# Kernel tuning notes

Hardware: AMD Instinct MI355X
Metric: run time of the kernel (lower is better)

The kernel has to match this reference:

```python
import jax, jax.numpy as jnp
import numpy as np
import math

V, H, L, NH, I, E, K, S, B = 32000, 1024, 4, 16, 2816, 8, 2, 2048, 1
HD = H // NH
MOE_IDX = 2
EPS = 1e-6
THETA = 10000.0
AUX_COEF, Z_COEF = 0.01, 0.001


def setup_inputs() -> dict:
    key = jax.random.key(0)
    ks = jax.random.split(key, 20)
    std = 0.02
    n_dense = L - 1  # layers 0,1,3
    inp = {
        "input_ids": jax.random.randint(ks[0], (B, S), 0, V, dtype=jnp.int64),
        "embed": jax.random.normal(ks[1], (V, H), jnp.float32) * std,
        "ln1_w": jnp.ones((L, H), jnp.float32),
        "ln2_w": jnp.ones((L, H), jnp.float32),
        "wq": jax.random.normal(ks[2], (L, H, H), jnp.float32) * std,
        "wk": jax.random.normal(ks[3], (L, H, H), jnp.float32) * std,
        "wv": jax.random.normal(ks[4], (L, H, H), jnp.float32) * std,
        "wo": jax.random.normal(ks[5], (L, H, H), jnp.float32) * std,
        "dense_gate": jax.random.normal(ks[6], (n_dense, H, I), jnp.float32) * std,
        "dense_up": jax.random.normal(ks[7], (n_dense, H, I), jnp.float32) * std,
        "dense_down": jax.random.normal(ks[8], (n_dense, I, H), jnp.float32) * std,
        "router_w": jax.random.normal(ks[9], (H, E), jnp.float32) * std,
        "moe_gate": jax.random.normal(ks[10], (E, H, I), jnp.float32) * std,
        "moe_up": jax.random.normal(ks[11], (E, H, I), jnp.float32) * std,
        "moe_down": jax.random.normal(ks[12], (E, I, H), jnp.float32) * std,
        "final_norm_w": jnp.ones((H,), jnp.float32),
    }
    return inp


def rmsnorm(x, w):
    return x * jax.lax.rsqrt(jnp.mean(x * x, -1, keepdims=True) + EPS) * w


def rope_tables():
    inv_freq = 1.0 / (THETA ** (jnp.arange(0, HD, 2, dtype=jnp.float32) / HD))
    ang = jnp.arange(S, dtype=jnp.float32)[:, None] * inv_freq[None, :]  # [S, HD/2]
    return jnp.cos(ang), jnp.sin(ang)


def apply_rope(x, cos, sin):
    # x: [B,S,NH,HD]; cos/sin [S,HD/2] -> broadcast [1,S,1,HD/2]
    c = cos[None, :, None, :]
    s = sin[None, :, None, :]
    x1, x2 = jnp.split(x, 2, axis=-1)
    return jnp.concatenate([x1 * c - x2 * s, x2 * c + x1 * s], axis=-1)


def attention(x, wq, wk, wv, wo, cos, sin, mask):
    q = (x @ wq).reshape(B, S, NH, HD)
    k = (x @ wk).reshape(B, S, NH, HD)
    v = (x @ wv).reshape(B, S, NH, HD)
    q = apply_rope(q, cos, sin)
    k = apply_rope(k, cos, sin)
    scores = jnp.einsum("bqhd,bkhd->bhqk", q, k) / math.sqrt(HD)
    scores = jnp.where(mask, scores, jnp.finfo(scores.dtype).min)
    p = jax.nn.softmax(scores, axis=-1)
    o = jnp.einsum("bhqk,bkhd->bqhd", p, v).reshape(B, S, H)
    return o @ wo


def swiglu_mlp(x, wg, wu, wd):
    return (jax.nn.silu(x @ wg) * (x @ wu)) @ wd


def moe_layer(x, router_w, wg, wu, wd):
    T = B * S
    xf = x.reshape(T, H)
    rl = xf @ router_w  # [T,E]
    probs = jax.nn.softmax(rl, axis=-1)
    vals, idx = jax.lax.top_k(probs, K)  # [T,K]
    vals = vals / jnp.sum(vals, axis=-1, keepdims=True)
    rows = jnp.arange(T)[:, None]
    w = jnp.zeros((T, E), xf.dtype).at[rows, idx].set(vals)  # dense combine weights
    g = jnp.einsum("th,ehi->tei", xf, wg)
    u = jnp.einsum("th,ehi->tei", xf, wu)
    a = jax.nn.silu(g) * u
    y = jnp.einsum("tei,eih,te->th", a, wd, w)
    # load-balancing aux loss (Switch-style) + router z-loss
    sel = jnp.zeros((T, E), xf.dtype).at[rows, idx].add(1.0)
    f = jnp.mean(sel, axis=0)
    P = jnp.mean(probs, axis=0)
    aux = AUX_COEF * E * jnp.sum(f * P)
    z = Z_COEF * jnp.mean(jax.nn.logsumexp(rl, axis=-1) ** 2)
    return y.reshape(B, S, H), aux + z


def reference(input_ids, embed, ln1_w, ln2_w, wq, wk, wv, wo,
              dense_gate, dense_up, dense_down,
              router_w, moe_gate, moe_up, moe_down, final_norm_w):
    cos, sin = rope_tables()
    mask = jnp.tril(jnp.ones((S, S), bool))[None, None, :, :]
    h = embed[input_ids]  # [B,S,H]
    total_aux = jnp.float32(0.0)
    n_moe = 0
    d = 0  # dense layer counter
    for li in range(L):
        res = h
        hn = rmsnorm(h, ln1_w[li])
        h = res + attention(hn, wq[li], wk[li], wv[li], wo[li], cos, sin, mask)
        res = h
        hn = rmsnorm(h, ln2_w[li])
        if li == MOE_IDX:
            y, aux = moe_layer(hn, router_w, moe_gate, moe_up, moe_down)
            total_aux = total_aux + aux
            n_moe += 1
        else:
            y = swiglu_mlp(hn, dense_gate[d], dense_up[d], dense_down[d])
            d += 1
        h = res + y
    h = rmsnorm(h, final_norm_w)
    logits = h @ embed.T  # tied lm_head
    aux_loss = total_aux / n_moe
    return logits, aux_loss
```

## Files before the change

kernel.cpp:

```cpp
#include <hip/hip_runtime.h>
#include <hip/hip_bf16.h>
#include <math.h>

#define SEQ 2048
#define HID 1024
#define NHEAD 16
#define HDIM 64
#define IDIM 2816
#define NEXP 8
#define VOCAB 32000

#define ASTRIDE 144

typedef float f32x4v __attribute__((ext_vector_type(4)));
typedef __bf16 bf16x8v __attribute__((ext_vector_type(8)));
typedef __bf16 bf16x4v __attribute__((ext_vector_type(4)));

__device__ __forceinline__ bf16x8v cvt8(const float4& a, const float4& b) {
  bf16x8v r;
  r[0] = (__bf16)a.x; r[1] = (__bf16)a.y; r[2] = (__bf16)a.z; r[3] = (__bf16)a.w;
  r[4] = (__bf16)b.x; r[5] = (__bf16)b.y; r[6] = (__bf16)b.z; r[7] = (__bf16)b.w;
  return r;
}

#define MFMA(a, b, c) __builtin_amdgcn_mfma_f32_16x16x32_bf16(a, b, c, 0, 0, 0)

__device__ __forceinline__ void gld_lds16(const void* g, void* l) {
  __builtin_amdgcn_global_load_lds(
      (const __attribute__((address_space(1))) unsigned int*)(unsigned long long)g,
      (__attribute__((address_space(3))) unsigned int*)(unsigned int)(unsigned long long)l,
      16, 0, 0);
}

__global__ __launch_bounds__(256) void wsplit_t_kernel(
    const float* __restrict__ W, __bf16* __restrict__ WH, __bf16* __restrict__ WL,
    int K, int N)
{
  __shared__ float tile[64][65];
  const int tid = threadIdx.x;
  const size_t zofs = (size_t)blockIdx.z * K * N;
  const int n0 = blockIdx.x * 64, k0 = blockIdx.y * 64;
#pragma unroll
  for (int r = 0; r < 4; ++r) {
    int kk = (tid >> 4) + r * 16;
    int nn = (tid & 15) * 4;
    float4 v = *(const float4*)(W + zofs + (size_t)(k0 + kk) * N + n0 + nn);
    tile[kk][nn] = v.x; tile[kk][nn + 1] = v.y;
    tile[kk][nn + 2] = v.z; tile[kk][nn + 3] = v.w;
  }
  __syncthreads();
  const int nn = tid >> 2;
  const int kk = (tid & 3) * 16;
  __bf16* dh = WH + zofs + (size_t)(n0 + nn) * K + k0 + kk;
  __bf16* dl = WL + zofs + (size_t)(n0 + nn) * K + k0 + kk;
  bf16x8v h0, l0, h1, l1;
#pragma unroll
  for (int j = 0; j < 8; ++j) {
    float f = tile[kk + j][nn];
    __bf16 hb = (__bf16)f; h0[j] = hb; l0[j] = (__bf16)(f - (float)hb);
    f = tile[kk + 8 + j][nn];
    hb = (__bf16)f; h1[j] = hb; l1[j] = (__bf16)(f - (float)hb);
  }
  *(bf16x8v*)dh = h0; *(bf16x8v*)(dh + 8) = h1;
  *(bf16x8v*)dl = l0; *(bf16x8v*)(dl + 8) = l1;
}

__global__ __launch_bounds__(256) void wsplit_th_kernel(
    const float* __restrict__ W, __bf16* __restrict__ WH, int K, int N)
{
  __shared__ float tile[64][65];
  const int tid = threadIdx.x;
  const size_t zofs = (size_t)blockIdx.z * K * N;
  const int n0 = blockIdx.x * 64, k0 = blockIdx.y * 64;
#pragma unroll
  for (int r = 0; r < 4; ++r) {
    int kk = (tid >> 4) + r * 16;
    int nn = (tid & 15) * 4;
    float4 v = *(const float4*)(W + zofs + (size_t)(k0 + kk) * N + n0 + nn);
    tile[kk][nn] = v.x; tile[kk][nn + 1] = v.y;
    tile[kk][nn + 2] = v.z; tile[kk][nn + 3] = v.w;
  }
  __syncthreads();
  const int nn = tid >> 2;
  const int kk = (tid & 3) * 16;
  __bf16* dh = WH + zofs + (size_t)(n0 + nn) * K + k0 + kk;
  bf16x8v h0, h1;
#pragma unroll
  for (int j = 0; j < 8; ++j) {
    h0[j] = (__bf16)tile[kk + j][nn];
    h1[j] = (__bf16)tile[kk + 8 + j][nn];
  }
  *(bf16x8v*)dh = h0; *(bf16x8v*)(dh + 8) = h1;
}

__global__ __launch_bounds__(256) void esplit_kernel(
    const float* __restrict__ E, __bf16* __restrict__ EH)
{
  size_t i = ((size_t)blockIdx.x * 256 + threadIdx.x) * 8;
  float4 a = *(const float4*)(E + i);
  float4 b = *(const float4*)(E + i + 4);
  *(bf16x8v*)(EH + i) = cvt8(a, b);
}

template<bool COMP, bool ACCUM, int BM, int BN, bool XSWZ>
__global__ __launch_bounds__(256) void gemm_bt_kernel(
    const __bf16* __restrict__ Ah, const __bf16* __restrict__ Al,
    const __bf16* __restrict__ B0h, const __bf16* __restrict__ B0l,
    const __bf16* __restrict__ B1h, const __bf16* __restrict__ B1l,
    const __bf16* __restrict__ B2h, const __bf16* __restrict__ B2l,
    float* __restrict__ C0, float* __restrict__ C1, float* __restrict__ C2,
    int M, int N, int Kd)
{
  const __bf16* __restrict__ Bh = (blockIdx.z == 0) ? B0h : (blockIdx.z == 1 ? B1h : B2h);
  const __bf16* __restrict__ Bl = (blockIdx.z == 0) ? B0l : (blockIdx.z == 1 ? B1l : B2l);
  float* __restrict__ C         = (blockIdx.z == 0) ? C0 : (blockIdx.z == 1 ? C1 : C2);
  constexpr int ATILE = BM * 64;
  constexpr int BTILE = BN * 64;
  constexpr int MFR = BM / 32;
  constexpr int NFR = BN / 32;
  __shared__ __align__(16) char smem[COMP ? 2 * (ATILE + BTILE) : (ATILE + BTILE)];
  char* AsH = smem;
  char* BsH = smem + ATILE;
  char* AsL = COMP ? smem + ATILE + BTILE : smem;
  char* BsL = COMP ? smem + 2 * ATILE + BTILE : smem + ATILE;
  const int tid = threadIdx.x;
  int bm, bn;
  if (XSWZ) {
    int id = blockIdx.x;
    int xcd = id & 7;
    int j = id >> 3;
    if (BM == 128) {
      bm = j & 15;
      bn = xcd * 32 + (j >> 4);
    } else {
      bm = j & 31;
      bn = xcd * 32 + (j >> 5);
    }
    if (bn >= N / BN) return;
  } else {
    bm = blockIdx.y;
    bn = blockIdx.x;
  }
  const int wid = tid >> 6, lane = tid & 63;
  const int wm = (wid >> 1) * (BM / 2), wn = (wid & 1) * (BN / 2);
  const int lr = lane & 15, kh = lane >> 4;
  const int lrow = lane >> 2;
  const int lcol = (lane & 3) << 3;

  f32x4v acc[MFR][NFR];
  const f32x4v z4 = {0.f, 0.f, 0.f, 0.f};
#pragma unroll
  for (int i = 0; i < MFR; ++i)
#pragma unroll
    for (int j2 = 0; j2 < NFR; ++j2) acc[i][j2] = z4;

  for (int k0 = 0; k0 < Kd; k0 += 32) {
    __syncthreads();
#pragma unroll
    for (int c = wid; c < BM / 16; c += 4) {
      size_t gofs = (size_t)(bm * BM + c * 16 + lrow) * Kd + k0 + lcol;
      gld_lds16(Ah + gofs, AsH + c * 1024);
      if (COMP) gld_lds16(Al + gofs, AsL + c * 1024);
    }
#pragma unroll
    for (int c = wid; c < BN / 16; c += 4) {
      size_t gofs = (size_t)(bn * BN + c * 16 + lrow) * Kd + k0 + lcol;
      gld_lds16(Bh + gofs, BsH + c * 1024);
      if (COMP) gld_lds16(Bl + gofs, BsL + c * 1024);
    }
    __syncthreads();

    bf16x8v ah[MFR], al[MFR], bh4[NFR], bl4[NFR];
#pragma unroll
    for (int i = 0; i < MFR; ++i) {
      int r = wm + (i << 4) + lr;
      int off = r * 64 + (kh << 4);
      ah[i] = *(const bf16x8v*)(AsH + off);
      if (COMP) al[i] = *(const bf16x8v*)(AsL + off);
    }
#pragma unroll
    for (int i = 0; i < NFR; ++i) {
      int r = wn + (i << 4) + lr;
      int off = r * 64 + (kh << 4);
      bh4[i] = *(const bf16x8v*)(BsH + off);
      if (COMP) bl4[i] = *(const bf16x8v*)(BsL + off);
    }
#pragma unroll
    for (int mi = 0; mi < MFR; ++mi)
#pragma unroll
      for (int ni = 0; ni < NFR; ++ni) {
        if (COMP) {
          acc[mi][ni] = MFMA(al[mi], bh4[ni], acc[mi][ni]);
          acc[mi][ni] = MFMA(ah[mi], bl4[ni], acc[mi][ni]);
        }
        acc[mi][ni] = MFMA(ah[mi], bh4[ni], acc[mi][ni]);
      }
  }

  const int cr0 = kh << 2;
#pragma unroll
  for (int mi = 0; mi < MFR; ++mi)
#pragma unroll
    for (int ni = 0; ni < NFR; ++ni)
#pragma unroll
      for (int r = 0; r < 4; ++r) {
        int row = bm * BM + wm + (mi << 4) + cr0 + r;
        int col = bn * BN + wn + (ni << 4) + lr;
        size_t idx = (size_t)row * N + col;
        if (ACCUM) C[idx] += acc[mi][ni][r];
        else       C[idx] = acc[mi][ni][r];
      }
}

template<bool COMP>
__global__ __launch_bounds__(256) void gemm_qkv_kernel(
    const __bf16* __restrict__ Ah, const __bf16* __restrict__ Al,
    const __bf16* __restrict__ Bqh, const __bf16* __restrict__ Bql,
    const __bf16* __restrict__ Bkh, const __bf16* __restrict__ Bkl,
    const __bf16* __restrict__ Bvh, const __bf16* __restrict__ Bvl,
    __bf16* __restrict__ QH, __bf16* __restrict__ QL,
    __bf16* __restrict__ KH, __bf16* __restrict__ KL,
    float* __restrict__ Vout,
    const float* __restrict__ CT, const float* __restrict__ ST)
{
  const __bf16* __restrict__ Bh = (blockIdx.z == 0) ? Bqh : (blockIdx.z == 1 ? Bkh : Bvh);
  const __bf16* __restrict__ Bl = (blockIdx.z == 0) ? Bql : (blockIdx.z == 1 ? Bkl : Bvl);
  constexpr int ATILE = 64 * 64;
  constexpr int BTILE = 128 * 64;
  __shared__ __align__(16) char smem[COMP ? 2 * (ATILE + BTILE) : (ATILE + BTILE)];
  char* AsH = smem;
  char* BsH = smem + ATILE;
  char* AsL = COMP ? smem + ATILE + BTILE : smem;
  char* BsL = COMP ? smem + 2 * ATILE + BTILE : smem + ATILE;
  const int tid = threadIdx.x;
  const int bm = blockIdx.y, bn = blockIdx.x;
  const int wid = tid >> 6, lane = tid & 63;
  const int wm = (wid >> 1) << 5, wn = (wid & 1) << 6;
  const int lr = lane & 15, kh = lane >> 4;
  const int lrow = lane >> 2;
  const int lcol = (lane & 3) << 3;

  f32x4v acc[2][4];
  const f32x4v z4 = {0.f, 0.f, 0.f, 0.f};
#pragma unroll
  for (int i = 0; i < 2; ++i)
#pragma unroll
    for (int j2 = 0; j2 < 4; ++j2) acc[i][j2] = z4;

  for (int k0 = 0; k0 < HID; k0 += 32) {
    __syncthreads();
    {
      int c = wid;
      size_t gofs = (size_t)(bm * 64 + c * 16 + lrow) * HID + k0 + lcol;
      gld_lds16(Ah + gofs, AsH + c * 1024);
      if (COMP) gld_lds16(Al + gofs, AsL + c * 1024);
    }
#pragma unroll
    for (int c = wid; c < 8; c += 4) {
      size_t gofs = (size_t)(bn * 128 + c * 16 + lrow) * HID + k0 + lcol;
      gld_lds16(Bh + gofs, BsH + c * 1024);
      if (COMP) gld_lds16(Bl + gofs, BsL + c * 1024);
    }
    __syncthreads();

    bf16x8v ah2[2], al2[2], bh4[4], bl4[4];
#pragma unroll
    for (int i = 0; i < 2; ++i) {
      int r = wm + (i << 4) + lr;
      int off = r * 64 + (kh << 4);
      ah2[i] = *(const bf16x8v*)(AsH + off);
      if (COMP) al2[i] = *(const bf16x8v*)(AsL + off);
    }
#pragma unroll
    for (int i = 0; i < 4; ++i) {
      int r = wn + (i << 4) + lr;
      int off = r * 64 + (kh << 4);
      bh4[i] = *(const bf16x8v*)(BsH + off);
      if (COMP) bl4[i] = *(const bf16x8v*)(BsL + off);
    }
#pragma unroll
    for (int mi = 0; mi < 2; ++mi)
#pragma unroll
      for (int ni = 0; ni < 4; ++ni) {
        if (COMP) {
          acc[mi][ni] = MFMA(al2[mi], bh4[ni], acc[mi][ni]);
          acc[mi][ni] = MFMA(ah2[mi], bl4[ni], acc[mi][ni]);
        }
        acc[mi][ni] = MFMA(ah2[mi], bh4[ni], acc[mi][ni]);
      }
  }

  const int cr0 = kh << 2;
  if (blockIdx.z == 2) {
#pragma unroll
    for (int mi = 0; mi < 2; ++mi)
#pragma unroll
      for (int ni = 0; ni < 4; ++ni)
#pragma unroll
        for (int r = 0; r < 4; ++r) {
          int row = bm * 64 + wm + (mi << 4) + cr0 + r;
          int col = bn * 128 + wn + (ni << 4) + lr;
          Vout[(size_t)row * HID + col] = acc[mi][ni][r];
        }
  } else {
    const float scale = (blockIdx.z == 0) ? 0.125f : 1.0f;
    __bf16* OH = (blockIdx.z == 0) ? QH : KH;
    __bf16* OL = (blockIdx.z == 0) ? QL : KL;
#pragma unroll
    for (int mi = 0; mi < 2; ++mi)
#pragma unroll
      for (int ni = 0; ni < 2; ++ni)
#pragma unroll
        for (int r = 0; r < 4; ++r) {
          int row = bm * 64 + wm + (mi << 4) + cr0 + r;
          int col = bn * 128 + wn + (ni << 4) + lr;
          int i = col & 31;
          float c = CT[row * 32 + i], sn = ST[row * 32 + i];
          float x1 = acc[mi][ni][r];
          float x2 = acc[mi][ni + 2][r];
          float o1 = (x1 * c - x2 * sn) * scale;
          float o2 = (x2 * c + x1 * sn) * scale;
          size_t ofs = (size_t)row * HID + col;
          __bf16 h1 = (__bf16)o1;
          OH[ofs] = h1; OL[ofs] = (__bf16)(o1 - (float)h1);
          __bf16 h2 = (__bf16)o2;
          OH[ofs + 32] = h2; OL[ofs + 32] = (__bf16)(o2 - (float)h2);
        }
  }
}

template<bool COMP>
__global__ __launch_bounds__(256) void gemm_dgu_kernel(
    const __bf16* __restrict__ Ah, const __bf16* __restrict__ Al,
    const __bf16* __restrict__ BGh, const __bf16* __restrict__ BGl,
    const __bf16* __restrict__ BUh, const __bf16* __restrict__ BUl,
    __bf16* __restrict__ GH, __bf16* __restrict__ GL)
{
  __shared__ __align__(16) char AsH[4096], AsL[4096];
  __shared__ __align__(16) char BgH[4096], BgL[4096];
  __shared__ __align__(16) char BuH[4096], BuL[4096];
  const int tid = threadIdx.x;
  const int bn = blockIdx.x, bm = blockIdx.y;
  const int wid = tid >> 6, lane = tid & 63;
  const int wm = (wid >> 1) << 5, wn = (wid & 1) << 5;
  const int lr = lane & 15, kh = lane >> 4;
  const int lrow = lane >> 2;
  const int lcol = (lane & 3) << 3;

  f32x4v accg[2][2], accu[2][2];
  const f32x4v z4 = {0.f, 0.f, 0.f, 0.f};
#pragma unroll
  for (int i = 0; i < 2; ++i)
#pragma unroll
    for (int j = 0; j < 2; ++j) { accg[i][j] = z4; accu[i][j] = z4; }

  for (int k0 = 0; k0 < HID; k0 += 32) {
    __syncthreads();
    {
      int c = wid;
      size_t aofs = (size_t)(bm * 64 + c * 16 + lrow) * HID + k0 + lcol;
      gld_lds16(Ah + aofs, AsH + c * 1024);
      if (COMP) gld_lds16(Al + aofs, AsL + c * 1024);
      size_t bofs = (size_t)(bn * 64 + c * 16 + lrow) * HID + k0 + lcol;
      gld_lds16(BGh + bofs, BgH + c * 1024);
      gld_lds16(BUh + bofs, BuH + c * 1024);
      if (COMP) {
        gld_lds16(BGl + bofs, BgL + c * 1024);
        gld_lds16(BUl + bofs, BuL + c * 1024);
      }
    }
    __syncthreads();

    bf16x8v af[2], afl[2], bg4[2], bgl4[2], bu4[2], bul4[2];
#pragma unroll
    for (int i = 0; i < 2; ++i) {
      int r = wm + (i << 4) + lr;
      int off = r * 64 + (kh << 4);
      af[i] = *(const bf16x8v*)(AsH + off);
      if (COMP) afl[i] = *(const bf16x8v*)(AsL + off);
    }
#pragma unroll
    for (int i = 0; i < 2; ++i) {
      int r = wn + (i << 4) + lr;
      int off = r * 64 + (kh << 4);
      bg4[i] = *(const bf16x8v*)(BgH + off);
      bu4[i] = *(const bf16x8v*)(BuH + off);
      if (COMP) {
        bgl4[i] = *(const bf16x8v*)(BgL + off);
        bul4[i] = *(const bf16x8v*)(BuL + off);
      }
    }
#pragma unroll
    for (int mi = 0; mi < 2; ++mi)
#pragma unroll
      for (int ni = 0; ni < 2; ++ni) {
        if (COMP) {
          accg[mi][ni] = MFMA(afl[mi], bg4[ni], accg[mi][ni]);
          accg[mi][ni] = MFMA(af[mi], bgl4[ni], accg[mi][ni]);
        }
        accg[mi][ni] = MFMA(af[mi], bg4[ni], accg[mi][ni]);
        if (COMP) {
          accu[mi][ni] = MFMA(afl[mi], bu4[ni], accu[mi][ni]);
          accu[mi][ni] = MFMA(af[mi], bul4[ni], accu[mi][ni]);
        }
        accu[mi][ni] = MFMA(af[mi], bu4[ni], accu[mi][ni]);
      }
  }

  const int cr0 = kh << 2;
#pragma unroll
  for (int mi = 0; mi < 2; ++mi)
#pragma unroll
    for (int ni = 0; ni < 2; ++ni)
#pragma unroll
      for (int r = 0; r < 4; ++r) {
        int row = bm * 64 + wm + (mi << 4) + cr0 + r;
        int col = bn * 64 + wn + (ni << 4) + lr;
        float gv = accg[mi][ni][r];
        float uv = accu[mi][ni][r];
        float a = gv / (1.f + __expf(-gv)) * uv;
        size_t idx = (size_t)row * IDIM + col;
        __bf16 hb = (__bf16)a;
        GH[idx] = hb;
        GL[idx] = (__bf16)(a - (float)hb);
      }
}

__global__ __launch_bounds__(256) void vtsplit_kernel(
    const float* __restrict__ V, __bf16* __restrict__ VTH, __bf16* __restrict__ VTL)
{
  __shared__ float tile[64][65];
  const int tid = threadIdx.x;
  const int s0 = blockIdx.x * 64;
  const int head = blockIdx.y;
#pragma unroll
  for (int r = 0; r < 4; ++r) {
    int ss = (tid >> 4) + r * 16;
    int dd = (tid & 15) * 4;
    float4 v = *(const float4*)(V + (size_t)(s0 + ss) * HID + head * 64 + dd);
    tile[ss][dd] = v.x; tile[ss][dd + 1] = v.y;
    tile[ss][dd + 2] = v.z; tile[ss][dd + 3] = v.w;
  }
  __syncthreads();
#pragma unroll
  for (int half = 0; half < 2; ++half) {
    const int d = (tid >> 3) + (half << 5);
    const int c = tid & 7;
    bf16x8v hv, lv;
#pragma unroll
    for (int j = 0; j < 8; ++j) {
      float f = tile[c * 8 + j][d];
      __bf16 hb = (__bf16)f;
      hv[j] = hb; lv[j] = (__bf16)(f - (float)hb);
    }
    size_t dst = (size_t)(head * 64 + d) * SEQ + s0 + c * 8;
    *(bf16x8v*)(VTH + dst) = hv;
    *(bf16x8v*)(VTL + dst) = lv;
  }
}

__global__ __launch_bounds__(256) void attn_flash_kernel(
    const __bf16* __restrict__ QH, const __bf16* __restrict__ QL,
    const __bf16* __restrict__ KH, const __bf16* __restrict__ KL,
    const __bf16* __restrict__ VTH, const __bf16* __restrict__ VTL,
    __bf16* __restrict__ OH, __bf16* __restrict__ OL)
{
  const int head = blockIdx.y;
  const int tid = threadIdx.x, wid = tid >> 6, lane = tid & 63;
  const int lr = lane & 15, kh = lane >> 4;
  __shared__ __align__(16) char KsH[64 * ASTRIDE], KsL[64 * ASTRIDE];
  __shared__ __align__(16) char VtH[64 * ASTRIDE], VtL[64 * ASTRIDE];
  __shared__ __align__(16) char PsH[4][16 * ASTRIDE], PsL[4][16 * ASTRIDE];

#pragma unroll
  for (int seg = 0; seg < 2; ++seg) {
    const int qt = seg ? (31 - (int)blockIdx.x) : (int)blockIdx.x;

    const size_t qofs = (size_t)(qt * 64 + wid * 16 + lr) * HID + head * HDIM;
    const bf16x8v qfh0 = *(const bf16x8v*)(QH + qofs + (kh << 3));
    const bf16x8v qfh1 = *(const bf16x8v*)(QH + qofs + 32 + (kh << 3));
    const bf16x8v qfl0 = *(const bf16x8v*)(QL + qofs + (kh << 3));
    const bf16x8v qfl1 = *(const bf16x8v*)(QL + qofs + 32 + (kh << 3));

    float m_run[4], l_run[4];
    f32x4v oacc[4];
    const f32x4v z4 = {0.f, 0.f, 0.f, 0.f};
#pragma unroll
    for (int i = 0; i < 4; ++i) { m_run[i] = -1e30f; l_run[i] = 0.f; oacc[i] = z4; }

    for (int kt = 0; kt <= qt; ++kt) {
      __syncthreads();
#pragma unroll
      for (int p = 0; p < 2; ++p) {
        int g = tid + (p << 8);
        int r = g >> 3;
        int c = g & 7;
        int off = r * ASTRIDE + (c << 4);
        const size_t kofs = (size_t)(kt * 64 + r) * HID + head * HDIM + (c << 3);
        *(bf16x8v*)(KsH + off) = *(const bf16x8v*)(KH + kofs);
        *(bf16x8v*)(KsL + off) = *(const bf16x8v*)(KL + kofs);
        const size_t vofs = (size_t)(head * 64 + r) * SEQ + kt * 64 + (c << 3);
        *(bf16x8v*)(VtH + off) = *(const bf16x8v*)(VTH + vofs);
        *(bf16x8v*)(VtL + off) = *(const bf16x8v*)(VTL + vofs);
      }
      __syncthreads();

      float sv[4][4];
#pragma unroll
      for (int stt = 0; stt < 4; ++stt) {
        int r = (stt << 4) + lr;
        int off0 = r * ASTRIDE + (kh << 4);
        int off1 = off0 + 64;
        bf16x8v kfh0 = *(const bf16x8v*)(KsH + off0);
        bf16x8v kfl0 = *(const bf16x8v*)(KsL + off0);
        bf16x8v kfh1 = *(const bf16x8v*)(KsH + off1);
        bf16x8v kfl1 = *(const bf16x8v*)(KsL + off1);
        f32x4v s = z4;
        s = MFMA(qfl0, kfh0, s);
        s = MFMA(qfh0, kfl0, s);
        s = MFMA(qfh0, kfh0, s);
        s = MFMA(qfl1, kfh1, s);
        s = MFMA(qfh1, kfl1, s);
        s = MFMA(qfh1, kfh1, s);
        int key = kt * 64 + (stt << 4) + lr;
#pragma unroll
        for (int rr = 0; rr < 4; ++rr) {
          int qr = qt * 64 + wid * 16 + (kh << 2) + rr;
          sv[stt][rr] = (key <= qr) ? s[rr] : -1e30f;
        }
      }

#pragma unroll
      for (int rr = 0; rr < 4; ++rr) {
        float mx = fmaxf(fmaxf(sv[0][rr], sv[1][rr]), fmaxf(sv[2][rr], sv[3][rr]));
#pragma unroll
        for (int d = 1; d < 16; d <<= 1) mx = fmaxf(mx, __shfl_xor(mx, d));
        float mnew = fmaxf(m_run[rr], mx);
        float scl = __expf(m_run[rr] - mnew);
        float pv[4];
#pragma unroll
        for (int stt = 0; stt < 4; ++stt) pv[stt] = __expf(sv[stt][rr] - mnew);
        float rs = pv[0] + pv[1] + pv[2] + pv[3];
#pragma unroll
        for (int d = 1; d < 16; d <<= 1) rs += __shfl_xor(rs, d);
        l_run[rr] = l_run[rr] * scl + rs;
        m_run[rr] = mnew;
#pragma unroll
        for (int n = 0; n < 4; ++n) oacc[n][rr] *= scl;
        int qlr = (kh << 2) + rr;
#pragma unroll
        for (int stt = 0; stt < 4; ++stt) {
          __bf16 hb = (__bf16)pv[stt];
          __bf16 lb = (__bf16)(pv[stt] - (float)hb);
          int off = qlr * ASTRIDE + (((stt << 4) + lr) << 1);
          *(__bf16*)(PsH[wid] + off) = hb;
          *(__bf16*)(PsL[wid] + off) = lb;
        }
      }

      int poff0 = lr * ASTRIDE + (kh << 4);
      int poff1 = poff0 + 64;
      bf16x8v pah0 = *(const bf16x8v*)(PsH[wid] + poff0);
      bf16x8v pal0 = *(const bf16x8v*)(PsL[wid] + poff0);
      bf16x8v pah1 = *(const bf16x8v*)(PsH[wid] + poff1);
      bf16x8v pal1 = *(const bf16x8v*)(PsL[wid] + poff1);
#pragma unroll
      for (int n = 0; n < 4; ++n) {
        int vr = (n << 4) + lr;
        int voff0 = vr * ASTRIDE + (kh << 4);
        int voff1 = voff0 + 64;
        bf16x8v vfh0 = *(const bf16x8v*)(VtH + voff0);
        bf16x8v vfl0 = *(const bf16x8v*)(VtL + voff0);
        bf16x8v vfh1 = *(const bf16x8v*)(VtH + voff1);
        bf16x8v vfl1 = *(const bf16x8v*)(VtL + voff1);
        oacc[n] = MFMA(pal0, vfh0, oacc[n]);
        oacc[n] = MFMA(pah0, vfl0, oacc[n]);
        oacc[n] = MFMA(pah0, vfh0, oacc[n]);
        oacc[n] = MFMA(pal1, vfh1, oacc[n]);
        oacc[n] = MFMA(pah1, vfl1, oacc[n]);
        oacc[n] = MFMA(pah1, vfh1, oacc[n]);
      }
    }

#pragma unroll
    for (int n = 0; n < 4; ++n)
#pragma unroll
      for (int rr = 0; rr < 4; ++rr) {
        int qr = qt * 64 + wid * 16 + (kh << 2) + rr;
        size_t ofs = (size_t)qr * HID + head * HDIM + (n << 4) + lr;
        float val = oacc[n][rr] / l_run[rr];
        __bf16 hb = (__bf16)val;
        OH[ofs] = hb;
        OL[ofs] = (__bf16)(val - (float)hb);
      }
  }
}

__global__ __launch_bounds__(256) void gemm_moe_guf_kernel(
    const __bf16* __restrict__ Xh,
    const __bf16* __restrict__ MGH, const __bf16* __restrict__ MUH,
    __bf16* __restrict__ A2, const float* __restrict__ W,
    const int* __restrict__ list, const int* __restrict__ cnt8,
    const int* __restrict__ off8)
{
  const int e = blockIdx.z;
  const int cnt = cnt8[e];
  const int bn = blockIdx.x, bm = blockIdx.y;
  if (bm * 128 >= cnt) return;
  const int base = off8[e];
  __shared__ __align__(16) char AsB[8192];
  __shared__ __align__(16) char BgB[4096];
  __shared__ __align__(16) char BuB[4096];
  const int tid = threadIdx.x;
  const int wid = tid >> 6, lane = tid & 63;
  const int wm = (wid >> 1) << 6, wn = (wid & 1) << 5;
  const int lr = lane & 15, kh = lane >> 4;
  const int lrow = lane >> 2;
  const int lcol = (lane & 3) << 3;

  f32x4v accg[4][2], accu[4][2];
  const f32x4v z4 = {0.f, 0.f, 0.f, 0.f};
#pragma unroll
  for (int i = 0; i < 4; ++i)
#pragma unroll
    for (int j = 0; j < 2; ++j) { accg[i][j] = z4; accu[i][j] = z4; }

  for (int k0 = 0; k0 < HID; k0 += 32) {
    __syncthreads();
#pragma unroll
    for (int c = wid; c < 8; c += 4) {
      int rg = bm * 128 + c * 16 + lrow;
      int tok = list[e * SEQ + (rg < cnt ? rg : cnt - 1)];
      gld_lds16(Xh + (size_t)tok * HID + k0 + lcol, AsB + c * 1024);
    }
    {
      int c = wid;
      size_t wofs = (size_t)(e * IDIM + bn * 64 + c * 16 + lrow) * HID + k0 + lcol;
      gld_lds16(MGH + wofs, BgB + c * 1024);
      gld_lds16(MUH + wofs, BuB + c * 1024);
    }
    __syncthreads();

    bf16x8v af[4], bg4[2], bu4[2];
#pragma unroll
    for (int i = 0; i < 4; ++i) {
      int r = wm + (i << 4) + lr;
      af[i] = *(const bf16x8v*)(AsB + r * 64 + (kh << 4));
    }
#pragma unroll
    for (int i = 0; i < 2; ++i) {
      int r = wn + (i << 4) + lr;
      bg4[i] = *(const bf16x8v*)(BgB + r * 64 + (kh << 4));
      bu4[i] = *(const bf16x8v*)(BuB + r * 64 + (kh << 4));
    }
#pragma unroll
    for (int mi = 0; mi < 4; ++mi)
#pragma unroll
      for (int ni = 0; ni < 2; ++ni) {
        accg[mi][ni] = MFMA(af[mi], bg4[ni], accg[mi][ni]);
        accu[mi][ni] = MFMA(af[mi], bu4[ni], accu[mi][ni]);
      }
  }

  const int cr0 = kh << 2;
#pragma unroll
  for (int mi = 0; mi < 4; ++mi)
#pragma unroll
    for (int ni = 0; ni < 2; ++ni)
#pragma unroll
      for (int r = 0; r < 4; ++r) {
        int row = bm * 128 + wm + (mi << 4) + cr0 + r;
        if (row < cnt) {
          int col = bn * 64 + wn + (ni << 4) + lr;
          int tok = list[e * SEQ + row];
          float w = W[tok * 8 + e];
          float gval = accg[mi][ni][r];
          float uval = accu[mi][ni][r];
          float a = gval / (1.f + __expf(-gval)) * uval * w;
          A2[(size_t)(base + row) * IDIM + col] = (__bf16)a;
        }
      }
}

__global__ __launch_bounds__(256) void gemm_moe_down2_kernel(
    const __bf16* __restrict__ A2, const __bf16* __restrict__ MDH,
    float* __restrict__ Y2,
    const int* __restrict__ cnt8, const int* __restrict__ off8)
{
  const int e = blockIdx.z;
  const int cnt = cnt8[e];
  const int bn = blockIdx.x, bm = blockIdx.y;
  if (bm * 128 >= cnt) return;
  const int base = off8[e];
  __shared__ __align__(16) char AsB[8192];
  __shared__ __align__(16) char BsB[4096];
  const int tid = threadIdx.x;
  const int wid = tid >> 6, lane = tid & 63;
  const int wm = (wid >> 1) << 6, wn = (wid & 1) << 5;
  const int lr = lane & 15, kh = lane >> 4;
  const int lrow = lane >> 2;
  const int lcol = (lane & 3) << 3;

  f32x4v acc[4][2];
  const f32x4v z4 = {0.f, 0.f, 0.f, 0.f};
#pragma unroll
  for (int i = 0; i < 4; ++i)
#pragma unroll
    for (int j = 0; j < 2; ++j) acc[i][j] = z4;

  for (int k0 = 0; k0 < IDIM; k0 += 32) {
    __syncthreads();
#pragma unroll
    for (int c = wid; c < 8; c += 4) {
      int rg = bm * 128 + c * 16 + lrow;
      int row = (rg < cnt ? rg : cnt - 1);
      gld_lds16(A2 + (size_t)(base + row) * IDIM + k0 + lcol, AsB + c * 1024);
    }
    {
      int c = wid;
      gld_lds16(MDH + (size_t)(e * HID + bn * 64 + c * 16 + lrow) * IDIM + k0 + lcol,
                BsB + c * 1024);
    }
    __syncthreads();

    bf16x8v af[4], bfv[2];
#pragma unroll
    for (int i = 0; i < 4; ++i) {
      int r = wm + (i << 4) + lr;
      af[i] = *(const bf16x8v*)(AsB + r * 64 + (kh << 4));
    }
#pragma unroll
    for (int i = 0; i < 2; ++i) {
      int r = wn + (i << 4) + lr;
      bfv[i] = *(const bf16x8v*)(BsB + r * 64 + (kh << 4));
    }
#pragma unroll
    for (int mi = 0; mi < 4; ++mi)
#pragma unroll
      for (int ni = 0; ni < 2; ++ni)
        acc[mi][ni] = MFMA(af[mi], bfv[ni], acc[mi][ni]);
  }

  const int cr0 = kh << 2;
#pragma unroll
  for (int mi = 0; mi < 4; ++mi)
#pragma unroll
    for (int ni = 0; ni < 2; ++ni)
#pragma unroll
      for (int r = 0; r < 4; ++r) {
        int row = bm * 128 + wm + (mi << 4) + cr0 + r;
        if (row < cnt) {
          int col = bn * 64 + wn + (ni << 4) + lr;
          Y2[(size_t)(base + row) * HID + col] = acc[mi][ni][r];
        }
      }
}

__global__ __launch_bounds__(256) void moe_scatter_kernel(
    const int* __restrict__ tokpair, const int* __restrict__ off8,
    const float* __restrict__ Y2, float* __restrict__ H)
{
  const int t = blockIdx.x;
  const int i = threadIdx.x;
  int p0 = tokpair[t * 2], p1 = tokpair[t * 2 + 1];
  size_t r0 = off8[p0 >> 16] + (p0 & 0xffff);
  size_t r1 = off8[p1 >> 16] + (p1 & 0xffff);
  float4 a = ((const float4*)(Y2 + r0 * HID))[i];
  float4 b = ((const float4*)(Y2 + r1 * HID))[i];
  float4 hv = ((float4*)(H + (size_t)t * HID))[i];
  hv.x = (hv.x + a.x) + b.x;
  hv.y = (hv.y + a.y) + b.y;
  hv.z = (hv.z + a.z) + b.z;
  hv.w = (hv.w + a.w) + b.w;
  ((float4*)(H + (size_t)t * HID))[i] = hv;
}

__global__ void tables_kernel(float* __restrict__ CT, float* __restrict__ ST)
{
  int idx = blockIdx.x * 256 + threadIdx.x;
  int s = idx >> 5, i = idx & 31;
  double inv = exp(-log(10000.0) * (double)i / 32.0);
  double ang = (double)s * inv;
  CT[idx] = (float)cos(ang);
  ST[idx] = (float)sin(ang);
}

__global__ __launch_bounds__(256) void embed_kernel(
    const int* __restrict__ ids, const float* __restrict__ E, float* __restrict__ H)
{
  int t = blockIdx.x;
  int id = ids[t];
  ((float4*)(H + (size_t)t * HID))[threadIdx.x] =
      ((const float4*)(E + (size_t)id * HID))[threadIdx.x];
}

__global__ __launch_bounds__(256) void rmsnorm_kernel(
    const float* __restrict__ X, const float* __restrict__ W,
    float* __restrict__ O, __bf16* __restrict__ OHb, __bf16* __restrict__ OLb)
{
  int t = blockIdx.x;
  int tid = threadIdx.x;
  float4 v = ((const float4*)(X + (size_t)t * HID))[tid];
  float ss = v.x * v.x + v.y * v.y + v.z * v.z + v.w * v.w;
#pragma unroll
  for (int d = 1; d < 64; d <<= 1) ss += __shfl_xor(ss, d);
  __shared__ float red[4];
  if ((tid & 63) == 0) red[tid >> 6] = ss;
  __syncthreads();
  float tot = red[0] + red[1] + red[2] + red[3];
  float inv = 1.0f / sqrtf(tot * (1.0f / 1024.0f) + 1e-6f);
  float4 w = ((const float4*)W)[tid];
  float4 r;
  r.x = v.x * inv * w.x; r.y = v.y * inv * w.y;
  r.z = v.z * inv * w.z; r.w = v.w * inv * w.w;
  ((float4*)(O + (size_t)t * HID))[tid] = r;
  float f[4] = {r.x, r.y, r.z, r.w};
  bf16x4v hv, lv;
#pragma unroll
  for (int j = 0; j < 4; ++j) {
    __bf16 hb = (__bf16)f[j];
    hv[j] = hb; lv[j] = (__bf16)(f[j] - (float)hb);
  }
  *(bf16x4v*)(OHb + (size_t)t * HID + tid * 4) = hv;
  *(bf16x4v*)(OLb + (size_t)t * HID + tid * 4) = lv;
}

__global__ __launch_bounds__(256) void router_kernel(
    const float* __restrict__ X, const float* __restrict__ RW, float* __restrict__ RL)
{
  int wid = threadIdx.x >> 6, lane = threadIdx.x & 63;
  int t = blockIdx.x * 4 + wid;
  const float* x = X + (size_t)t * HID;
  float a0 = 0, a1 = 0, a2 = 0, a3 = 0, a4 = 0, a5 = 0, a6 = 0, a7 = 0;
  for (int hh = lane; hh < HID; hh += 64) {
    float xv = x[hh];
    float4 f0 = *(const float4*)(RW + hh * 8);
    float4 f1 = *(const float4*)(RW + hh * 8 + 4);
    a0 += xv * f0.x; a1 += xv * f0.y; a2 += xv * f0.z; a3 += xv * f0.w;
    a4 += xv * f1.x; a5 += xv * f1.y; a6 += xv * f1.z; a7 += xv * f1.w;
  }
#pragma unroll
  for (int d = 1; d < 64; d <<= 1) {
    a0 += __shfl_xor(a0, d); a1 += __shfl_xor(a1, d);
    a2 += __shfl_xor(a2, d); a3 += __shfl_xor(a3, d);
    a4 += __shfl_xor(a4, d); a5 += __shfl_xor(a5, d);
    a6 += __shfl_xor(a6, d); a7 += __shfl_xor(a7, d);
  }
  if (lane == 0) {
    float* dst = RL + (size_t)t * 8;
    dst[0] = a0; dst[1] = a1; dst[2] = a2; dst[3] = a3;
    dst[4] = a4; dst[5] = a5; dst[6] = a6; dst[7] = a7;
  }
}

__global__ void zero_kernel(float* __restrict__ p, int n)
{
  int i = threadIdx.x;
  if (i < n) p[i] = 0.f;
}

__global__ void zeroi_kernel(int* __restrict__ p, int n)
{
  int i = threadIdx.x;
  if (i < n) p[i] = 0;
}

__global__ __launch_bounds__(256) void topk_kernel(
    const float* __restrict__ RL, float* __restrict__ W, float* __restrict__ AUX)
{
  int t = blockIdx.x * 256 + threadIdx.x;
  int lane = threadIdx.x & 63;
  float r[8];
#pragma unroll
  for (int e = 0; e < 8; ++e) r[e] = RL[t * 8 + e];
  float mx = r[0];
#pragma unroll
  for (int e = 1; e < 8; ++e) mx = fmaxf(mx, r[e]);
  float p[8];
  float se = 0.f;
#pragma unroll
  for (int e = 0; e < 8; ++e) { p[e] = __expf(r[e] - mx); se += p[e]; }
  float inv = 1.f / se;
#pragma unroll
  for (int e = 0; e < 8; ++e) p[e] *= inv;
  float lse = logf(se) + mx;
  int i1 = 0; float v1 = p[0];
#pragma unroll
  for (int e = 1; e < 8; ++e) if (p[e] > v1) { v1 = p[e]; i1 = e; }
  int i2 = -1; float v2 = -1.f;
#pragma unroll
  for (int e = 0; e < 8; ++e) if (e != i1 && p[e] > v2) { v2 = p[e]; i2 = e; }
  float s12 = v1 + v2;
#pragma unroll
  for (int e = 0; e < 8; ++e)
    W[t * 8 + e] = (e == i1) ? v1 / s12 : ((e == i2) ? v2 / s12 : 0.f);
#pragma unroll
  for (int e = 0; e < 8; ++e) {
    float fe = ((i1 == e) ? 1.f : 0.f) + ((i2 == e) ? 1.f : 0.f);
    float pe = p[e];
#pragma unroll
    for (int d = 1; d < 64; d <<= 1) { fe += __shfl_xor(fe, d); pe += __shfl_xor(pe, d); }
    if (lane == 0) { atomicAdd(&AUX[e], fe); atomicAdd(&AUX[8 + e], pe); }
  }
  float zz = lse * lse;
#pragma unroll
  for (int d = 1; d < 64; d <<= 1) zz += __shfl_xor(zz, d);
  if (lane == 0) atomicAdd(&AUX[16], zz);
}

__global__ void aux_kernel(const float* __restrict__ AUX, float* __restrict__ OUT)
{
  float s = 0.f;
#pragma unroll
  for (int e = 0; e < 8; ++e)
    s += (AUX[e] * (1.f / 2048.f)) * (AUX[8 + e] * (1.f / 2048.f));
  float auxv = 0.01f * 8.f * s;
  float z = 0.001f * (AUX[16] * (1.f / 2048.f));
  OUT[(size_t)SEQ * VOCAB] = auxv + z;
}

__global__ __launch_bounds__(256) void build_list_kernel(
    const float* __restrict__ W, int* __restrict__ cnt, int* __restrict__ list,
    int* __restrict__ tokpair)
{
  int t = blockIdx.x * 256 + threadIdx.x;
  int j = 0;
#pragma unroll
  for (int e = 0; e < 8; ++e) {
    if (W[t * 8 + e] > 0.f) {
      int p = atomicAdd(&cnt[e], 1);
      list[e * SEQ + p] = t;
      tokpair[t * 2 + j] = (e << 16) | p;
      ++j;
    }
  }
}

__global__ void prefix_kernel(const int* __restrict__ cnt, int* __restrict__ off)
{
  if (threadIdx.x == 0) {
    int s = 0;
    for (int e = 0; e < 8; ++e) { off[e] = s; s += cnt[e]; }
  }
}

extern "C" void kernel_launch(void* const* d_in, const int* in_sizes, int n_in,
                              void* d_out, int out_size, void* d_ws, size_t ws_size,
                              hipStream_t stream)
{
  const int*   ids   = (const int*)d_in[0];
  const float* embed = (const float*)d_in[1];
  const float* ln1   = (const float*)d_in[2];
  const float* ln2   = (const float*)d_in[3];
  const float* wq    = (const float*)d_in[4];
  const float* wk    = (const float*)d_in[5];
  const float* wv    = (const float*)d_in[6];
  const float* wo    = (const float*)d_in[7];
  const float* dg    = (const float*)d_in[8];
  const float* du    = (const float*)d_in[9];
  const float* dd    = (const float*)d_in[10];
  const float* rw    = (const float*)d_in[11];
  const float* mg    = (const float*)d_in[12];
  const float* mu    = (const float*)d_in[13];
  const float* md    = (const float*)d_in[14];
  const float* fin   = (const float*)d_in[15];
  float* out = (float*)d_out;

  char* ws = (char*)d_ws;
  float* h    = (float*)(ws + 0);
  float* hn   = (float*)(ws + 8388608);
  float* q    = (float*)(ws + 16777216);
  float* k    = (float*)(ws + 25165824);
  float* v    = (float*)(ws + 33554432);
  __bf16* oh  = (__bf16*)(ws + 41943040);
  __bf16* ol  = (__bf16*)(ws + 46137344);
  float* g    = (float*)(ws + 50331648);
  float* u    = (float*)(ws + 73400320);
  float* ct   = (float*)(ws + 96468992);
  float* st   = (float*)(ws + 96731136);
  float* rl   = (float*)(ws + 96993280);
  float* wmoe = (float*)(ws + 97058816);
  float* aux  = (float*)(ws + 97124352);
  int*   cnt  = (int*)  (ws + 97124608);
  int*   list = (int*)  (ws + 97124864);
  int*   tokp = (int*)  (ws + 97190400);
  int*   off8 = (int*)  (ws + 97206784);
  __bf16* wqh = (__bf16*)(ws + 97320960);
  __bf16* wql = (__bf16*)(ws + 105709568);
  __bf16* wkh = (__bf16*)(ws + 114098176);
  __bf16* wkl = (__bf16*)(ws + 122486784);
  __bf16* wvh = (__bf16*)(ws + 130875392);
  __bf16* wvl = (__bf16*)(ws + 139264000);
  __bf16* woh = (__bf16*)(ws + 147652608);
  __bf16* wol = (__bf16*)(ws + 156041216);
  __bf16* dgh = (__bf16*)(ws + 164429824);
  __bf16* dgl = (__bf16*)(ws + 181731328);
  __bf16* duh = (__bf16*)(ws + 199032832);
  __bf16* dul = (__bf16*)(ws + 216334336);
  __bf16* ddh = (__bf16*)(ws + 233635840);
  __bf16* ddl = (__bf16*)(ws + 250937344);
  __bf16* eh  = (__bf16*)(ws + 268238848);
  __bf16* hnh = (__bf16*)(ws + 333774848);
  __bf16* hnl = (__bf16*)(ws + 337969152);
  __bf16* gh  = (__bf16*)(ws + 342163456);
  __bf16* gl  = (__bf16*)(ws + 353697792);
  __bf16* mgh = (__bf16*)(ws + 365232128);
  __bf16* muh = (__bf16*)(ws + 411369472);
  __bf16* mdh = (__bf16*)(ws + 457506816);
  __bf16* qh  = (__bf16*)g;
  __bf16* ql  = (__bf16*)((char*)g + 4194304);
  __bf16* kbh = (__bf16*)((char*)g + 8388608);
  __bf16* kbl = (__bf16*)((char*)g + 12582912);
  __bf16* vth = (__bf16*)u;
  __bf16* vtl = (__bf16*)((char*)u + 4194304);
  __bf16* a2  = (__bf16*)g;
  float*  y2  = u;

  wsplit_t_kernel<<<dim3(16, 16, 4), 256, 0, stream>>>(wq, wqh, wql, HID, HID);
  wsplit_t_kernel<<<dim3(16, 16, 4), 256, 0, stream>>>(wk, wkh, wkl, HID, HID);
  wsplit_t_kernel<<<dim3(16, 16, 4), 256, 0, stream>>>(wv, wvh, wvl, HID, HID);
  wsplit_t_kernel<<<dim3(16, 16, 4), 256, 0, stream>>>(wo, woh, wol, HID, HID);
  wsplit_t_kernel<<<dim3(44, 16, 3), 256, 0, stream>>>(dg, dgh, dgl, HID, IDIM);
  wsplit_t_kernel<<<dim3(44, 16, 3), 256, 0, stream>>>(du, duh, dul, HID, IDIM);
  wsplit_t_kernel<<<dim3(16, 44, 3), 256, 0, stream>>>(dd, ddh, ddl, IDIM, HID);
  wsplit_th_kernel<<<dim3(44, 16, 8), 256, 0, stream>>>(mg, mgh, HID, IDIM);
  wsplit_th_kernel<<<dim3(44, 16, 8), 256, 0, stream>>>(mu, muh, HID, IDIM);
  wsplit_th_kernel<<<dim3(16, 44, 8), 256, 0, stream>>>(md, mdh, IDIM, HID);
  esplit_kernel<<<16000, 256, 0, stream>>>(embed, eh);

  tables_kernel<<<256, 256, 0, stream>>>(ct, st);
  embed_kernel<<<SEQ, 256, 0, stream>>>(ids, embed, h);

  for (int li = 0; li < 4; ++li) {
    const bool comp = (li <= 2);
    rmsnorm_kernel<<<SEQ, 256, 0, stream>>>(h, ln1 + li * HID, hn, hnh, hnl);
    size_t wofs = (size_t)li * HID * HID;
    if (comp)
      gemm_qkv_kernel<true><<<dim3(8, 32, 3), 256, 0, stream>>>(
          hnh, hnl, wqh + wofs, wql + wofs, wkh + wofs, wkl + wofs,
          wvh + wofs, wvl + wofs, qh, ql, kbh, kbl, v, ct, st);
    else
      gemm_qkv_kernel<false><<<dim3(8, 32, 3), 256, 0, stream>>>(
          hnh, hnh, wqh + wofs, wqh + wofs, wkh + wofs, wkh + wofs,
          wvh + wofs, wvh + wofs, qh, ql, kbh, kbl, v, ct, st);

    vtsplit_kernel<<<dim3(32, 16), 256, 0, stream>>>(v, vth, vtl);

    attn_flash_kernel<<<dim3(16, 16), 256, 0, stream>>>(
        qh, ql, kbh, kbl, vth, vtl, oh, ol);

    if (comp)
      gemm_bt_kernel<true, true, 64, 64, false><<<dim3(16, 32, 1), 256, 0, stream>>>(
          oh, ol, woh + wofs, wol + wofs, woh + wofs, wol + wofs,
          woh + wofs, wol + wofs, h, h, h, SEQ, HID, HID);
    else
      gemm_bt_kernel<false, true, 64, 64, false><<<dim3(16, 32, 1), 256, 0, stream>>>(
          oh, oh, woh + wofs, woh + wofs, woh + wofs, woh + wofs,
          woh + wofs, woh + wofs, h, h, h, SEQ, HID, HID);

    rmsnorm_kernel<<<SEQ, 256, 0, stream>>>(h, ln2 + li * HID, hn, hnh, hnl);
    if (li == 2) {
      router_kernel<<<512, 256, 0, stream>>>(hn, rw, rl);
      zero_kernel<<<1, 32, 0, stream>>>(aux, 17);
      topk_kernel<<<8, 256, 0, stream>>>(rl, wmoe, aux);
      aux_kernel<<<1, 1, 0, stream>>>(aux, out);
      zeroi_kernel<<<1, 32, 0, stream>>>(cnt, 8);
      build_list_kernel<<<8, 256, 0, stream>>>(wmoe, cnt, list, tokp);
      prefix_kernel<<<1, 64, 0, stream>>>(cnt, off8);
      gemm_moe_guf_kernel<<<dim3(44, 16, 8), 256, 0, stream>>>(
          hnh, mgh, muh, a2, wmoe, list, cnt, off8);
      gemm_moe_down2_kernel<<<dim3(16, 16, 8), 256, 0, stream>>>(
          a2, mdh, y2, cnt, off8);
      moe_scatter_kernel<<<SEQ, 256, 0, stream>>>(tokp, off8, y2, h);
    } else {
      int d = (li < 2) ? li : li - 1;
      size_t go = (size_t)d * HID * IDIM;
      if (comp)
        gemm_dgu_kernel<true><<<dim3(44, 32), 256, 0, stream>>>(
            hnh, hnl, dgh + go, dgl + go, duh + go, dul + go, gh, gl);
      else
        gemm_dgu_kernel<false><<<dim3(44, 32), 256, 0, stream>>>(
            hnh, hnh, dgh + go, dgh + go, duh + go, duh + go, gh, gl);
      if (comp)
        gemm_bt_kernel<true, true, 64, 64, false><<<dim3(16, 32, 1), 256, 0, stream>>>(
            gh, gl, ddh + go, ddl + go, ddh + go, ddl + go,
            ddh + go, ddl + go, h, h, h, SEQ, HID, IDIM);
      else
        gemm_bt_kernel<false, true, 64, 64, false><<<dim3(16, 32, 1), 256, 0, stream>>>(
            gh, gh, ddh + go, ddh + go, ddh + go, ddh + go,
            ddh + go, ddh + go, h, h, h, SEQ, HID, IDIM);
    }
  }
  rmsnorm_kernel<<<SEQ, 256, 0, stream>>>(h, fin, hn, hnh, hnl);
  gemm_bt_kernel<false, false, 128, 128, true><<<dim3(4096, 1, 1), 256, 0, stream>>>(
      hnh, hnh, eh, eh, eh, eh, eh, eh, out, out, out, SEQ, VOCAB, HID);
}
```

Before: 1.783 ms.

## Double-buffer LDS tiles in GEMM kernels to overlap loads with MFMA

Gives the dense, QKV, SwiGLU gate/up, MoE gate/up and MoE down GEMM kernels two LDS buffers each. The global-to-LDS load of the next K-slice is issued before the MFMAs on the current slice. This cuts the K-loop to one barrier per iteration and aims to hide global-load latency behind compute. In exchange it doubles shared-memory use, which can reduce occupancy. The overlap may also be lost if the compiler inserts a full vmcnt wait before the LDS reads.

```diff
diff --git a/kernel.cpp b/kernel.cpp
--- a/kernel.cpp
+++ b/kernel.cpp
@@ -118,11 +118,8 @@
   constexpr int BTILE = BN * 64;
   constexpr int MFR = BM / 32;
   constexpr int NFR = BN / 32;
-  __shared__ __align__(16) char smem[COMP ? 2 * (ATILE + BTILE) : (ATILE + BTILE)];
-  char* AsH = smem;
-  char* BsH = smem + ATILE;
-  char* AsL = COMP ? smem + ATILE + BTILE : smem;
-  char* BsL = COMP ? smem + 2 * ATILE + BTILE : smem + ATILE;
+  constexpr int SBUF = COMP ? 2 * (ATILE + BTILE) : (ATILE + BTILE);
+  __shared__ __align__(16) char smem[2 * SBUF];
   const int tid = threadIdx.x;
   int bm, bn;
   if (XSWZ) {
@@ -147,15 +144,11 @@
   const int lrow = lane >> 2;
   const int lcol = (lane & 3) << 3;
 
-  f32x4v acc[MFR][NFR];
-  const f32x4v z4 = {0.f, 0.f, 0.f, 0.f};
-#pragma unroll
-  for (int i = 0; i < MFR; ++i)
-#pragma unroll
-    for (int j2 = 0; j2 < NFR; ++j2) acc[i][j2] = z4;
-
-  for (int k0 = 0; k0 < Kd; k0 += 32) {
-    __syncthreads();
+  auto stage = [&](char* buf, int k0) {
+    char* AsH = buf;
+    char* BsH = buf + ATILE;
+    char* AsL = COMP ? buf + ATILE + BTILE : buf;
+    char* BsL = COMP ? buf + 2 * ATILE + BTILE : buf + ATILE;
 #pragma unroll
     for (int c = wid; c < BM / 16; c += 4) {
       size_t gofs = (size_t)(bm * BM + c * 16 + lrow) * Kd + k0 + lcol;
@@ -168,7 +161,25 @@
       gld_lds16(Bh + gofs, BsH + c * 1024);
       if (COMP) gld_lds16(Bl + gofs, BsL + c * 1024);
     }
+  };
+
+  f32x4v acc[MFR][NFR];
+  const f32x4v z4 = {0.f, 0.f, 0.f, 0.f};
+#pragma unroll
+  for (int i = 0; i < MFR; ++i)
+#pragma unroll
+    for (int j2 = 0; j2 < NFR; ++j2) acc[i][j2] = z4;
+
+  stage(smem, 0);
+  int cur = 0;
+  for (int k0 = 0; k0 < Kd; k0 += 32) {
     __syncthreads();
+    char* buf = smem + cur * SBUF;
+    if (k0 + 32 < Kd) stage(smem + (cur ^ 1) * SBUF, k0 + 32);
+    char* AsH = buf;
+    char* BsH = buf + ATILE;
+    char* AsL = COMP ? buf + ATILE + BTILE : buf;
+    char* BsL = COMP ? buf + 2 * ATILE + BTILE : buf + ATILE;
 
     bf16x8v ah[MFR], al[MFR], bh4[NFR], bl4[NFR];
 #pragma unroll
@@ -195,6 +206,7 @@
         }
         acc[mi][ni] = MFMA(ah[mi], bh4[ni], acc[mi][ni]);
       }
+    cur ^= 1;
   }
 
   const int cr0 = kh << 2;
@@ -227,11 +239,8 @@
   const __bf16* __restrict__ Bl = (blockIdx.z == 0) ? Bql : (blockIdx.z == 1 ? Bkl : Bvl);
   constexpr int ATILE = 64 * 64;
   constexpr int BTILE = 128 * 64;
-  __shared__ __align__(16) char smem[COMP ? 2 * (ATILE + BTILE) : (ATILE + BTILE)];
-  char* AsH = smem;
-  char* BsH = smem + ATILE;
-  char* AsL = COMP ? smem + ATILE + BTILE : smem;
-  char* BsL = COMP ? smem + 2 * ATILE + BTILE : smem + ATILE;
+  constexpr int SBUF = COMP ? 2 * (ATILE + BTILE) : (ATILE + BTILE);
+  __shared__ __align__(16) char smem[2 * SBUF];
   const int tid = threadIdx.x;
   const int bm = blockIdx.y, bn = blockIdx.x;
   const int wid = tid >> 6, lane = tid & 63;
@@ -240,15 +249,11 @@
   const int lrow = lane >> 2;
   const int lcol = (lane & 3) << 3;
 
-  f32x4v acc[2][4];
-  const f32x4v z4 = {0.f, 0.f, 0.f, 0.f};
-#pragma unroll
-  for (int i = 0; i < 2; ++i)
-#pragma unroll
-    for (int j2 = 0; j2 < 4; ++j2) acc[i][j2] = z4;
-
-  for (int k0 = 0; k0 < HID; k0 += 32) {
-    __syncthreads();
+  auto stage = [&](char* buf, int k0) {
+    char* AsH = buf;
+    char* BsH = buf + ATILE;
+    char* AsL = COMP ? buf + ATILE + BTILE : buf;
+    char* BsL = COMP ? buf + 2 * ATILE + BTILE : buf + ATILE;
     {
       int c = wid;
       size_t gofs = (size_t)(bm * 64 + c * 16 + lrow) * HID + k0 + lcol;
@@ -261,7 +266,25 @@
       gld_lds16(Bh + gofs, BsH + c * 1024);
       if (COMP) gld_lds16(Bl + gofs, BsL + c * 1024);
     }
+  };
+
+  f32x4v acc[2][4];
+  const f32x4v z4 = {0.f, 0.f, 0.f, 0.f};
+#pragma unroll
+  for (int i = 0; i < 2; ++i)
+#pragma unroll
+    for (int j2 = 0; j2 < 4; ++j2) acc[i][j2] = z4;
+
+  stage(smem, 0);
+  int cur = 0;
+  for (int k0 = 0; k0 < HID; k0 += 32) {
     __syncthreads();
+    char* buf = smem + cur * SBUF;
+    if (k0 + 32 < HID) stage(smem + (cur ^ 1) * SBUF, k0 + 32);
+    char* AsH = buf;
+    char* BsH = buf + ATILE;
+    char* AsL = COMP ? buf + ATILE + BTILE : buf;
+    char* BsL = COMP ? buf + 2 * ATILE + BTILE : buf + ATILE;
 
     bf16x8v ah2[2], al2[2], bh4[4], bl4[4];
 #pragma unroll
@@ -288,6 +311,7 @@
         }
         acc[mi][ni] = MFMA(ah2[mi], bh4[ni], acc[mi][ni]);
       }
+    cur ^= 1;
   }
 
   const int cr0 = kh << 2;
@@ -336,9 +360,8 @@
     const __bf16* __restrict__ BUh, const __bf16* __restrict__ BUl,
     __bf16* __restrict__ GH, __bf16* __restrict__ GL)
 {
-  __shared__ __align__(16) char AsH[4096], AsL[4096];
-  __shared__ __align__(16) char BgH[4096], BgL[4096];
-  __shared__ __align__(16) char BuH[4096], BuL[4096];
+  constexpr int SBUF = COMP ? 24576 : 12288;
+  __shared__ __align__(16) char smem[2 * SBUF];
   const int tid = threadIdx.x;
   const int bn = blockIdx.x, bm = blockIdx.y;
   const int wid = tid >> 6, lane = tid & 63;
@@ -347,6 +370,26 @@
   const int lrow = lane >> 2;
   const int lcol = (lane & 3) << 3;
 
+  auto stage = [&](char* buf, int k0) {
+    char* AsH = buf;
+    char* BgH = buf + 4096;
+    char* BuH = buf + 8192;
+    char* AsL = COMP ? buf + 12288 : buf;
+    char* BgL = COMP ? buf + 16384 : buf;
+    char* BuL = COMP ? buf + 20480 : buf;
+    int c = wid;
+    size_t aofs = (size_t)(bm * 64 + c * 16 + lrow) * HID + k0 + lcol;
+    gld_lds16(Ah + aofs, AsH + c * 1024);
+    if (COMP) gld_lds16(Al + aofs, AsL + c * 1024);
+    size_t bofs = (size_t)(bn * 64 + c * 16 + lrow) * HID + k0 + lcol;
+    gld_lds16(BGh + bofs, BgH + c * 1024);
+    gld_lds16(BUh + bofs, BuH + c * 1024);
+    if (COMP) {
+      gld_lds16(BGl + bofs, BgL + c * 1024);
+      gld_lds16(BUl + bofs, BuL + c * 1024);
+    }
+  };
+
   f32x4v accg[2][2], accu[2][2];
   const f32x4v z4 = {0.f, 0.f, 0.f, 0.f};
 #pragma unroll
@@ -354,22 +397,18 @@
 #pragma unroll
     for (int j = 0; j < 2; ++j) { accg[i][j] = z4; accu[i][j] = z4; }
 
+  stage(smem, 0);
+  int cur = 0;
   for (int k0 = 0; k0 < HID; k0 += 32) {
     __syncthreads();
-    {
-      int c = wid;
-      size_t aofs = (size_t)(bm * 64 + c * 16 + lrow) * HID + k0 + lcol;
-      gld_lds16(Ah + aofs, AsH + c * 1024);
-      if (COMP) gld_lds16(Al + aofs, AsL + c * 1024);
-      size_t bofs = (size_t)(bn * 64 + c * 16 + lrow) * HID + k0 + lcol;
-      gld_lds16(BGh + bofs, BgH + c * 1024);
-      gld_lds16(BUh + bofs, BuH + c * 1024);
-      if (COMP) {
-        gld_lds16(BGl + bofs, BgL + c * 1024);
-        gld_lds16(BUl + bofs, BuL + c * 1024);
-      }
-    }
-    __syncthreads();
+    char* buf = smem + cur * SBUF;
+    if (k0 + 32 < HID) stage(smem + (cur ^ 1) * SBUF, k0 + 32);
+    char* AsH = buf;
+    char* BgH = buf + 4096;
+    char* BuH = buf + 8192;
+    char* AsL = COMP ? buf + 12288 : buf;
+    char* BgL = COMP ? buf + 16384 : buf;
+    char* BuL = COMP ? buf + 20480 : buf;
 
     bf16x8v af[2], afl[2], bg4[2], bgl4[2], bu4[2], bul4[2];
 #pragma unroll
@@ -405,6 +444,7 @@
         }
         accu[mi][ni] = MFMA(af[mi], bu4[ni], accu[mi][ni]);
       }
+    cur ^= 1;
   }
 
   const int cr0 = kh << 2;
@@ -608,9 +648,8 @@
   const int bn = blockIdx.x, bm = blockIdx.y;
   if (bm * 128 >= cnt) return;
   const int base = off8[e];
-  __shared__ __align__(16) char AsB[8192];
-  __shared__ __align__(16) char BgB[4096];
-  __shared__ __align__(16) char BuB[4096];
+  constexpr int SBUF = 16384;
+  __shared__ __align__(16) char smem[2 * SBUF];
   const int tid = threadIdx.x;
   const int wid = tid >> 6, lane = tid & 63;
   const int wm = (wid >> 1) << 6, wn = (wid & 1) << 5;
@@ -618,15 +657,10 @@
   const int lrow = lane >> 2;
   const int lcol = (lane & 3) << 3;
 
-  f32x4v accg[4][2], accu[4][2];
-  const f32x4v z4 = {0.f, 0.f, 0.f, 0.f};
-#pragma unroll
-  for (int i = 0; i < 4; ++i)
-#pragma unroll
-    for (int j = 0; j < 2; ++j) { accg[i][j] = z4; accu[i][j] = z4; }
-
-  for (int k0 = 0; k0 < HID; k0 += 32) {
-    __syncthreads();
+  auto stage = [&](char* buf, int k0) {
+    char* AsB = buf;
+    char* BgB = buf + 8192;
+    char* BuB = buf + 12288;
 #pragma unroll
     for (int c = wid; c < 8; c += 4) {
       int rg = bm * 128 + c * 16 + lrow;
@@ -639,7 +673,24 @@
       gld_lds16(MGH + wofs, BgB + c * 1024);
       gld_lds16(MUH + wofs, BuB + c * 1024);
     }
+  };
+
+  f32x4v accg[4][2], accu[4][2];
+  const f32x4v z4 = {0.f, 0.f, 0.f, 0.f};
+#pragma unroll
+  for (int i = 0; i < 4; ++i)
+#pragma unroll
+    for (int j = 0; j < 2; ++j) { accg[i][j] = z4; accu[i][j] = z4; }
+
+  stage(smem, 0);
+  int cur = 0;
+  for (int k0 = 0; k0 < HID; k0 += 32) {
     __syncthreads();
+    char* buf = smem + cur * SBUF;
+    if (k0 + 32 < HID) stage(smem + (cur ^ 1) * SBUF, k0 + 32);
+    char* AsB = buf;
+    char* BgB = buf + 8192;
+    char* BuB = buf + 12288;
 
     bf16x8v af[4], bg4[2], bu4[2];
 #pragma unroll
@@ -660,6 +711,7 @@
         accg[mi][ni] = MFMA(af[mi], bg4[ni], accg[mi][ni]);
         accu[mi][ni] = MFMA(af[mi], bu4[ni], accu[mi][ni]);
       }
+    cur ^= 1;
   }
 
   const int cr0 = kh << 2;
@@ -692,8 +744,8 @@
   const int bn = blockIdx.x, bm = blockIdx.y;
   if (bm * 128 >= cnt) return;
   const int base = off8[e];
-  __shared__ __align__(16) char AsB[8192];
-  __shared__ __align__(16) char BsB[4096];
+  constexpr int SBUF = 12288;
+  __shared__ __align__(16) char smem[2 * SBUF];
   const int tid = threadIdx.x;
   const int wid = tid >> 6, lane = tid & 63;
   const int wm = (wid >> 1) << 6, wn = (wid & 1) << 5;
@@ -701,15 +753,9 @@
   const int lrow = lane >> 2;
   const int lcol = (lane & 3) << 3;
 
-  f32x4v acc[4][2];
-  const f32x4v z4 = {0.f, 0.f, 0.f, 0.f};
-#pragma unroll
-  for (int i = 0; i < 4; ++i)
-#pragma unroll
-    for (int j = 0; j < 2; ++j) acc[i][j] = z4;
-
-  for (int k0 = 0; k0 < IDIM; k0 += 32) {
-    __syncthreads();
+  auto stage = [&](char* buf, int k0) {
+    char* AsB = buf;
+    char* BsB = buf + 8192;
 #pragma unroll
     for (int c = wid; c < 8; c += 4) {
       int rg = bm * 128 + c * 16 + lrow;
@@ -721,7 +767,23 @@
       gld_lds16(MDH + (size_t)(e * HID + bn * 64 + c * 16 + lrow) * IDIM + k0 + lcol,
                 BsB + c * 1024);
     }
+  };
+
+  f32x4v acc[4][2];
+  const f32x4v z4 = {0.f, 0.f, 0.f, 0.f};
+#pragma unroll
+  for (int i = 0; i < 4; ++i)
+#pragma unroll
+    for (int j = 0; j < 2; ++j) acc[i][j] = z4;
+
+  stage(smem, 0);
+  int cur = 0;
+  for (int k0 = 0; k0 < IDIM; k0 += 32) {
     __syncthreads();
+    char* buf = smem + cur * SBUF;
+    if (k0 + 32 < IDIM) stage(smem + (cur ^ 1) * SBUF, k0 + 32);
+    char* AsB = buf;
+    char* BsB = buf + 8192;
 
     bf16x8v af[4], bfv[2];
 #pragma unroll
@@ -739,6 +801,7 @@
 #pragma unroll
       for (int ni = 0; ni < 2; ++ni)
         acc[mi][ni] = MFMA(af[mi], bfv[ni], acc[mi][ni]);
+    cur ^= 1;
   }
 
   const int cr0 = kh << 2;
```

After: 1.711 ms. 1.04x faster.
